# Optimization experiments

Measured on AMD Instinct MI355X. Metric: run time of the kernel, lower is better.

## Reference

```python
import jax, jax.numpy as jnp
import numpy as np

B, D, NUM_HOP, NUM_REL = 8192, 512, 8, 2000  # batch, input_dim, num_hop, num_relation
TAU = 1.0


def setup_inputs() -> dict:
    key = jax.random.key(0)
    ks = jax.random.split(key, 7)
    s = 1.0 / np.sqrt(D)  # PyTorch GRU uniform init bound
    return {
        "query": jax.random.normal(ks[0], (B, D), jnp.float32),
        "W_ih": jax.random.uniform(ks[1], (3 * D, D), jnp.float32, -s, s),
        "W_hh": jax.random.uniform(ks[2], (3 * D, D), jnp.float32, -s, s),
        "b_ih": jax.random.uniform(ks[3], (3 * D,), jnp.float32, -s, s),
        "b_hh": jax.random.uniform(ks[4], (3 * D,), jnp.float32, -s, s),
        "relation": jax.random.normal(ks[5], (2 * NUM_REL, D), jnp.float32),
        "eos": jax.random.normal(ks[6], (1, D), jnp.float32),
    }


def gru_cell(x, h, W_ih, W_hh, b_ih, b_hh):
    # PyTorch nn.GRU cell, gate order (r, z, n)
    gi = x @ W_ih.T + b_ih  # [B, 3D]
    gh = h @ W_hh.T + b_hh  # [B, 3D]
    ir, iz, i_n = jnp.split(gi, 3, axis=-1)
    hr, hz, h_n = jnp.split(gh, 3, axis=-1)
    r = jax.nn.sigmoid(ir + hr)
    z = jax.nn.sigmoid(iz + hz)
    n = jnp.tanh(i_n + r * h_n)
    return (1.0 - z) * n + z * h


def reference(query, W_ih, W_hh, b_ih, b_hh, relation, eos):
    # gru over seq [query, eos] starting from h0 = 0; hidden[1:] == final hx for 1 layer
    h0 = jnp.zeros_like(query)
    h1 = gru_cell(query, h0, W_ih, W_hh, b_ih, b_hh)
    hidden = gru_cell(jnp.broadcast_to(eos, query.shape), h1, W_ih, W_hh, b_ih, b_hh)

    def step(h, _):
        score = jnp.einsum('bd,rd->br', h, relation)          # [B, 2R]
        attention = jax.nn.softmax(score / TAU, axis=-1)
        subgoal = jnp.einsum('br,rd->bd', attention, relation)  # [B, D]
        h_new = gru_cell(subgoal, h, W_ih, W_hh, b_ih, b_hh)
        return h_new, subgoal

    _, subgoals = jax.lax.scan(step, hidden, None, length=NUM_HOP)  # [NUM_HOP, B, D]
    subgoals = jnp.moveaxis(subgoals, 0, 1)  # [B, NUM_HOP, D]
    masks = jnp.ones(subgoals.shape[:-1], dtype=bool)
    return subgoals, masks
```

## Files before the change

### kernel.cpp

```cpp
#include <hip/hip_runtime.h>


typedef _Float16 f16;
typedef _Float16 f16x8 __attribute__((ext_vector_type(8)));
typedef _Float16 f16x4 __attribute__((ext_vector_type(4)));
typedef float    f32x4 __attribute__((ext_vector_type(4)));

constexpr int BATCH = 8192;
constexpr int DDIM  = 512;
constexpr int D3    = 1536;
constexpr int NRELT = 4000;
constexpr int NRELP = 4096;
constexpr int NHOP  = 8;

#define MFMA16(a,b,c) __builtin_amdgcn_mfma_f32_16x16x32_f16((a),(b),(c),0,0,0)
#define BAR()   __builtin_amdgcn_s_barrier()
#define FENCE() asm volatile("" ::: "memory")
#define SCHED0() __builtin_amdgcn_sched_barrier(0)
#define VM(n) asm volatile("s_waitcnt vmcnt(" #n ")" ::: "memory")

__device__ __forceinline__ void gll16(const void* g, void* l) {
  __builtin_amdgcn_global_load_lds(
      (const __attribute__((address_space(1))) unsigned int*)g,
      (__attribute__((address_space(3))) unsigned int*)l, 16, 0, 0);
}

__global__ __launch_bounds__(256) void k_split(const float* __restrict__ src,
                                               f16* __restrict__ hi, f16* __restrict__ lo, int n) {
  int i = blockIdx.x * 256 + threadIdx.x;
  if (i >= n) return;
  float v = src[i];
  f16 h = (f16)v;
  hi[i] = h;
  lo[i] = (f16)(v - (float)h);
}

__global__ __launch_bounds__(256) void k_prep_rel(const float* __restrict__ rel,
    f16* __restrict__ rhi, f16* __restrict__ rlo,
    f16* __restrict__ thi, f16* __restrict__ tlo) {
  int i = blockIdx.x * 256 + threadIdx.x;
  if (i >= NRELP * DDIM) return;
  int r = i >> 9, d = i & 511;
  float v = (r < NRELT) ? rel[i] : 0.f;
  f16 h = (f16)v, l = (f16)(v - (float)h);
  rhi[i] = h; rlo[i] = l;
  thi[(size_t)d * NRELP + r] = h;
  tlo[(size_t)d * NRELP + r] = l;
}

__global__ __launch_bounds__(64) void k_gieos(const float* __restrict__ W,
                                              const float* __restrict__ eos,
                                              float* __restrict__ out) {
  int o = blockIdx.x;
  float s = 0.f;
  for (int i = threadIdx.x; i < DDIM; i += 64) s += W[(size_t)o * DDIM + i] * eos[i];
  for (int off = 32; off; off >>= 1) s += __shfl_xor(s, off);
  if (threadIdx.x == 0) out[o] = s;
}

template<int EPI>
__device__ __forceinline__ void gemm_core(
    const f16* __restrict__ Ahi, const f16* __restrict__ Alo, int lda,
    const f16* __restrict__ Bhi, const f16* __restrict__ Blo, int ldb,
    float* __restrict__ Cout, f16* __restrict__ Chi, f16* __restrict__ Clo,
    int ldc, int m0, int n0, int kst, int nt, f16* lds)
{
  const int tid  = threadIdx.x;
  const int lane = tid & 63;
  const int wave = tid >> 6;
  const int wm = wave >> 2;
  const int wn = wave & 3;
  const int rb = lane & 15;
  const int sl = lane >> 4;
  const int srow = lane >> 2;

  auto stage2 = [&](int buf, int p, int k0) {
    const f16* src = (p == 0) ? Ahi : (p == 1) ? Alo : (p == 2) ? Bhi : Blo;
    const int ld   = (p < 2) ? lda : ldb;
    const int base = (p < 2) ? m0 : n0;
    f16* pl = lds + ((buf * 4 + p) << 13);
    #pragma unroll
    for (int c = 0; c < 2; ++c) {
      const int r0 = wave * 16 + c * 128;
      const int lr = r0 + srow;
      const int slot = (lane & 3) ^ ((lr >> 1) & 3);
      gll16(src + (size_t)(base + lr) * ld + k0 + slot * 8, pl + r0 * 32);
    }
  };
  auto rd = [&](int buf, int p, int lr) -> f16x8 {
    const int off = lr * 64 + ((sl ^ ((lr >> 1) & 3)) << 4);
    return *(const f16x8*)((const char*)(lds + ((buf * 4 + p) << 13)) + off);
  };

  stage2(0, 0, kst); stage2(0, 2, kst); stage2(0, 1, kst); stage2(0, 3, kst);

  f32x4 acc[8][4] = {};
  f16x8 ah[8], al[8], bh[4], bl[4];
  const int A0 = wm * 128, B0 = wn * 64;

  for (int t = 0; t < nt; ++t) {
    const int cur = t & 1;
    const int nxt = cur ^ 1;
    const bool more = (t + 1 < nt);
    const int kn = kst + (t + 1) * 32;

    if (more) { stage2(nxt, 0, kn); stage2(nxt, 2, kn); VM(8); } else { VM(4); }
    BAR(); FENCE();
    #pragma unroll
    for (int f = 0; f < 8; ++f) ah[f] = rd(cur, 0, A0 + f * 16 + rb);
    #pragma unroll
    for (int f = 0; f < 4; ++f) bh[f] = rd(cur, 2, B0 + f * 16 + rb);
    __builtin_amdgcn_s_setprio(1);
    #pragma unroll
    for (int m = 0; m < 8; ++m)
      #pragma unroll
      for (int n = 0; n < 4; ++n)
        acc[m][n] = MFMA16(ah[m], bh[n], acc[m][n]);
    __builtin_amdgcn_s_setprio(0);
    SCHED0();

    if (more) { stage2(nxt, 1, kn); VM(8); } else { VM(2); }
    BAR(); FENCE();
    #pragma unroll
    for (int f = 0; f < 8; ++f) al[f] = rd(cur, 1, A0 + f * 16 + rb);
    __builtin_amdgcn_s_setprio(1);
    #pragma unroll
    for (int m = 0; m < 8; ++m)
      #pragma unroll
      for (int n = 0; n < 4; ++n)
        acc[m][n] = MFMA16(al[m], bh[n], acc[m][n]);
    __builtin_amdgcn_s_setprio(0);
    SCHED0();

    if (more) { stage2(nxt, 3, kn); VM(8); } else { VM(0); }
    BAR(); FENCE();
    #pragma unroll
    for (int f = 0; f < 4; ++f) bl[f] = rd(cur, 3, B0 + f * 16 + rb);
    __builtin_amdgcn_s_setprio(1);
    #pragma unroll
    for (int m = 0; m < 8; ++m)
      #pragma unroll
      for (int n = 0; n < 4; ++n)
        acc[m][n] = MFMA16(ah[m], bl[n], acc[m][n]);
    __builtin_amdgcn_s_setprio(0);
    SCHED0();
  }

  #pragma unroll
  for (int fm = 0; fm < 8; ++fm)
    #pragma unroll
    for (int fn = 0; fn < 4; ++fn)
      #pragma unroll
      for (int r = 0; r < 4; ++r) {
        const int gr = m0 + wm * 128 + fm * 16 + sl * 4 + r;
        const int gc = n0 + wn * 64 + fn * 16 + rb;
        const float v = acc[fm][fn][r];
        if constexpr (EPI == 0) {
          Cout[(size_t)gr * ldc + gc] = v;
        } else {
          const f16 vh = (f16)v;
          Chi[(size_t)gr * ldc + gc] = vh;
          Clo[(size_t)gr * ldc + gc] = (f16)(v - (float)vh);
        }
      }
}

template<int EPI, int TM, int TN>
__global__ __launch_bounds__(512, 2)
void k_gemm8(const f16* __restrict__ Ahi, const f16* __restrict__ Alo, int lda,
             const f16* __restrict__ Bhi, const f16* __restrict__ Blo, int ldb,
             float* __restrict__ Cout, f16* __restrict__ Chi, f16* __restrict__ Clo,
             int ldc, int K, int gy)
{
  __shared__ __align__(16) f16 lds[2 * 4 * 256 * 32];
  const int bid = blockIdx.x;
  const int xcd = bid & 7;
  const int j   = bid >> 3;
  const int within = j % (TM * TN);
  const int st  = xcd + 8 * (j / (TM * TN));
  const int nl  = within / TM;
  const int r   = within % TM;
  const int gmx = 32 / TM;
  const int gmn = gy / TN;
  const int z   = st / (gmx * gmn);
  const int rem = st % (gmx * gmn);
  const int bn  = rem / gmx;
  const int bm  = rem % gmx;
  const int m = bm * TM + r;
  const int n = bn * TN + nl;
  float* Co = Cout ? Cout + (size_t)z * BATCH * (size_t)ldc : nullptr;
  gemm_core<EPI>(Ahi, Alo, lda, Bhi, Blo, ldb, Co, Chi, Clo, ldc,
                 m * 256, n * 256, z * K, K / 32, lds);
}

__global__ __launch_bounds__(512, 2)
void k_gemm8_gru(const f16* __restrict__ xhi, const f16* __restrict__ xlo,
                 const f16* __restrict__ hhi, const f16* __restrict__ hlo,
                 const f16* __restrict__ wihhi, const f16* __restrict__ wihlo,
                 const f16* __restrict__ whhhi, const f16* __restrict__ whhlo,
                 float* __restrict__ gi, float* __restrict__ gh)
{
  __shared__ __align__(16) f16 lds[2 * 4 * 256 * 32];
  const int bid = blockIdx.x;
  const int xcd = bid & 7;
  const int j   = bid >> 3;
  const int nl  = j / 8;
  const int r   = j % 8;
  const int bn  = xcd / 4;
  const int bm  = xcd % 4;
  const int m   = bm * 8 + r;
  const int nn  = bn * 6 + nl;
  const bool second = nn >= 6;
  gemm_core<0>(second ? hhi : xhi, second ? hlo : xlo, DDIM,
               second ? whhhi : wihhi, second ? whhlo : wihlo, DDIM,
               second ? gh : gi, nullptr, nullptr, D3,
               m * 256, (second ? nn - 6 : nn) * 256, 0, DDIM / 32, lds);
}

__global__ __launch_bounds__(256)
void k_softmax(f16* __restrict__ Shi, f16* __restrict__ Slo) {
  const int row = blockIdx.x;
  f16* phi = Shi + (size_t)row * NRELP;
  f16* plo = Slo + (size_t)row * NRELP;
  const int tid = threadIdx.x, lane = tid & 63, wv = tid >> 6;
  const int ng = (tid < 232) ? 4 : 3;
  f32x4 v[4];
  float mx = -3.402823e38f;
  #pragma unroll
  for (int i = 0; i < 4; ++i)
    if (i < ng) {
      f16x4 hv = *(const f16x4*)(phi + (tid + 256 * i) * 4);
      f16x4 lv = *(const f16x4*)(plo + (tid + 256 * i) * 4);
      #pragma unroll
      for (int j = 0; j < 4; ++j) v[i][j] = (float)hv[j] + (float)lv[j];
      mx = fmaxf(fmaxf(fmaxf(mx, v[i][0]), fmaxf(v[i][1], v[i][2])), v[i][3]);
    }
  float l = 0.f;
  #pragma unroll
  for (int i = 0; i < 4; ++i)
    if (i < ng)
      l += __expf(v[i][0] - mx) + __expf(v[i][1] - mx)
         + __expf(v[i][2] - mx) + __expf(v[i][3] - mx);
  #pragma unroll
  for (int off = 1; off < 64; off <<= 1) {
    float om = __shfl_xor(mx, off), ol = __shfl_xor(l, off);
    float nm = fmaxf(mx, om);
    l = l * __expf(mx - nm) + ol * __expf(om - nm);
    mx = nm;
  }
  __shared__ float sm[4], slr[4];
  if (lane == 0) { sm[wv] = mx; slr[wv] = l; }
  __syncthreads();
  const float fm = fmaxf(fmaxf(sm[0], sm[1]), fmaxf(sm[2], sm[3]));
  const float fl = slr[0] * __expf(sm[0] - fm) + slr[1] * __expf(sm[1] - fm)
                 + slr[2] * __expf(sm[2] - fm) + slr[3] * __expf(sm[3] - fm);
  const float il = 1.f / fl;
  #pragma unroll
  for (int i = 0; i < 4; ++i)
    if (i < ng) {
      f16x4 oh, ol;
      #pragma unroll
      for (int j = 0; j < 4; ++j) {
        const float pv = __expf(v[i][j] - fm) * il;
        const f16 ph = (f16)pv;
        oh[j] = ph;
        ol[j] = (f16)(pv - (float)ph);
      }
      *(f16x4*)(phi + (tid + 256 * i) * 4) = oh;
      *(f16x4*)(plo + (tid + 256 * i) * 4) = ol;
    }
  if (tid < 24) {
    f16x4 z = {(f16)0.f, (f16)0.f, (f16)0.f, (f16)0.f};
    *(f16x4*)(phi + (1000 + tid) * 4) = z;
    *(f16x4*)(plo + (1000 + tid) * 4) = z;
  }
}

__global__ __launch_bounds__(256)
void k_subred(const float* __restrict__ Cp, float* __restrict__ outp,
              f16* __restrict__ xhi, f16* __restrict__ xlo, int hop) {
  const int idx = blockIdx.x * 256 + threadIdx.x;
  const int b = idx >> 7, d4 = (idx & 127) * 4;
  const size_t o = (size_t)b * DDIM + d4;
  f32x4 s = *(const f32x4*)(Cp + o);
  s += *(const f32x4*)(Cp + (size_t)BATCH * DDIM + o);
  s += *(const f32x4*)(Cp + 2 * (size_t)BATCH * DDIM + o);
  s += *(const f32x4*)(Cp + 3 * (size_t)BATCH * DDIM + o);
  *(f32x4*)(outp + (size_t)b * (NHOP * DDIM) + (size_t)hop * DDIM + d4) = s;
  f16x4 vh, vl;
  #pragma unroll
  for (int j = 0; j < 4; ++j) {
    const f16 ph = (f16)s[j];
    vh[j] = ph;
    vl[j] = (f16)(s[j] - (float)ph);
  }
  *(f16x4*)(xhi + o) = vh;
  *(f16x4*)(xlo + o) = vl;
}

__global__ __launch_bounds__(256)
void k_gates(const float* __restrict__ gi, const float* __restrict__ givec,
             const float* __restrict__ gh,
             const float* __restrict__ bih, const float* __restrict__ bhh,
             const float* __restrict__ hin, float* __restrict__ hout,
             f16* __restrict__ hhi, f16* __restrict__ hlo)
{
  const int idx = blockIdx.x * 256 + threadIdx.x;
  const int b  = idx >> 7;
  const int d4 = (idx & 127) * 4;
  f32x4 ir, iz, inn;
  if (gi) {
    const float* g = gi + (size_t)b * D3 + d4;
    ir  = *(const f32x4*)(g);
    iz  = *(const f32x4*)(g + DDIM);
    inn = *(const f32x4*)(g + 2 * DDIM);
  } else {
    ir  = *(const f32x4*)(givec + d4);
    iz  = *(const f32x4*)(givec + DDIM + d4);
    inn = *(const f32x4*)(givec + 2 * DDIM + d4);
  }
  ir  += *(const f32x4*)(bih + d4);
  iz  += *(const f32x4*)(bih + DDIM + d4);
  inn += *(const f32x4*)(bih + 2 * DDIM + d4);
  f32x4 hr = {0.f, 0.f, 0.f, 0.f}, hz = {0.f, 0.f, 0.f, 0.f}, hn = {0.f, 0.f, 0.f, 0.f};
  if (gh) {
    const float* g = gh + (size_t)b * D3 + d4;
    hr = *(const f32x4*)(g);
    hz = *(const f32x4*)(g + DDIM);
    hn = *(const f32x4*)(g + 2 * DDIM);
  }
  hr += *(const f32x4*)(bhh + d4);
  hz += *(const f32x4*)(bhh + DDIM + d4);
  hn += *(const f32x4*)(bhh + 2 * DDIM + d4);
  f32x4 hp = {0.f, 0.f, 0.f, 0.f};
  if (hin) hp = *(const f32x4*)(hin + (size_t)b * DDIM + d4);
  f32x4 hv; f16x4 vh, vl;
  #pragma unroll
  for (int j = 0; j < 4; ++j) {
    const float r = 1.f / (1.f + __expf(-(ir[j] + hr[j])));
    const float z = 1.f / (1.f + __expf(-(iz[j] + hz[j])));
    const float n = tanhf(inn[j] + r * hn[j]);
    const float h = (1.f - z) * n + z * hp[j];
    hv[j] = h;
    const f16 ph = (f16)h;
    vh[j] = ph;
    vl[j] = (f16)(h - (float)ph);
  }
  *(f32x4*)(hout + (size_t)b * DDIM + d4) = hv;
  *(f16x4*)(hhi + (size_t)b * DDIM + d4) = vh;
  *(f16x4*)(hlo + (size_t)b * DDIM + d4) = vl;
}

__global__ __launch_bounds__(256) void k_ones(float* __restrict__ o, int n) {
  int i = blockIdx.x * 256 + threadIdx.x;
  if (i < n) o[i] = 1.0f;
}

extern "C" void kernel_launch(void* const* d_in, const int* in_sizes, int n_in,
                              void* d_out, int out_size, void* d_ws, size_t ws_size,
                              hipStream_t stream)
{
  const float* query = (const float*)d_in[0];
  const float* W_ih  = (const float*)d_in[1];
  const float* W_hh  = (const float*)d_in[2];
  const float* b_ih  = (const float*)d_in[3];
  const float* b_hh  = (const float*)d_in[4];
  const float* rel   = (const float*)d_in[5];
  const float* eos   = (const float*)d_in[6];
  float* out = (float*)d_out;
  (void)in_sizes; (void)n_in; (void)out_size; (void)ws_size;

  char* w = (char*)d_ws;
  f16* SPhi    = (f16*)w;   w += (size_t)BATCH * NRELP * 2;
  f16* SPlo    = (f16*)w;   w += (size_t)BATCH * NRELP * 2;
  float* Cpart = (float*)w; w += (size_t)4 * BATCH * DDIM * 4;
  float* hbuf  = (float*)w; w += (size_t)BATCH * DDIM * 4;
  f16* h_hi    = (f16*)w;   w += (size_t)BATCH * DDIM * 2;
  f16* h_lo    = (f16*)w;   w += (size_t)BATCH * DDIM * 2;
  f16* x_hi    = (f16*)w;   w += (size_t)BATCH * DDIM * 2;
  f16* x_lo    = (f16*)w;   w += (size_t)BATCH * DDIM * 2;
  f16* wih_hi  = (f16*)w;   w += (size_t)D3 * DDIM * 2;
  f16* wih_lo  = (f16*)w;   w += (size_t)D3 * DDIM * 2;
  f16* whh_hi  = (f16*)w;   w += (size_t)D3 * DDIM * 2;
  f16* whh_lo  = (f16*)w;   w += (size_t)D3 * DDIM * 2;
  f16* rel_hi  = (f16*)w;   w += (size_t)NRELP * DDIM * 2;
  f16* rel_lo  = (f16*)w;   w += (size_t)NRELP * DDIM * 2;
  f16* relT_hi = (f16*)w;   w += (size_t)DDIM * NRELP * 2;
  f16* relT_lo = (f16*)w;   w += (size_t)DDIM * NRELP * 2;
  float* gieos = (float*)w; w += (size_t)D3 * 4;
  float* gi = (float*)SPhi;
  float* gh = (float*)SPhi + (size_t)BATCH * D3;

  k_split<<<(BATCH * DDIM + 255) / 256, 256, 0, stream>>>(query, x_hi, x_lo, BATCH * DDIM);
  k_split<<<(D3 * DDIM + 255) / 256, 256, 0, stream>>>(W_ih, wih_hi, wih_lo, D3 * DDIM);
  k_split<<<(D3 * DDIM + 255) / 256, 256, 0, stream>>>(W_hh, whh_hi, whh_lo, D3 * DDIM);
  k_prep_rel<<<(NRELP * DDIM + 255) / 256, 256, 0, stream>>>(rel, rel_hi, rel_lo, relT_hi, relT_lo);
  k_gieos<<<D3, 64, 0, stream>>>(W_ih, eos, gieos);

  const int ggrid = BATCH * DDIM / 4 / 256;

  k_gemm8<0, 4, 6><<<192, 512, 0, stream>>>(x_hi, x_lo, DDIM, wih_hi, wih_lo, DDIM,
      gi, nullptr, nullptr, D3, DDIM, 6);
  k_gates<<<ggrid, 256, 0, stream>>>(gi, nullptr, nullptr, b_ih, b_hh, nullptr, hbuf, h_hi, h_lo);

  k_gemm8<0, 4, 6><<<192, 512, 0, stream>>>(h_hi, h_lo, DDIM, whh_hi, whh_lo, DDIM,
      gh, nullptr, nullptr, D3, DDIM, 6);
  k_gates<<<ggrid, 256, 0, stream>>>(nullptr, gieos, gh, b_ih, b_hh, hbuf, hbuf, h_hi, h_lo);

  for (int hop = 0; hop < NHOP; ++hop) {
    k_gemm8<1, 8, 8><<<512, 512, 0, stream>>>(h_hi, h_lo, DDIM, rel_hi, rel_lo, DDIM,
        nullptr, SPhi, SPlo, NRELP, DDIM, 16);
    k_softmax<<<BATCH, 256, 0, stream>>>(SPhi, SPlo);
    k_gemm8<0, 8, 2><<<256, 512, 0, stream>>>(SPhi, SPlo, NRELP,
        relT_hi, relT_lo, NRELP, Cpart, nullptr, nullptr, DDIM, 1024, 2);
    k_subred<<<ggrid, 256, 0, stream>>>(Cpart, out, x_hi, x_lo, hop);
    k_gemm8_gru<<<384, 512, 0, stream>>>(x_hi, x_lo, h_hi, h_lo,
        wih_hi, wih_lo, whh_hi, whh_lo, gi, gh);
    k_gates<<<ggrid, 256, 0, stream>>>(gi, nullptr, gh, b_ih, b_hh, hbuf, hbuf, h_hi, h_lo);
  }

  k_ones<<<(BATCH * NHOP + 255) / 256, 256, 0, stream>>>(out + (size_t)BATCH * NHOP * DDIM, BATCH * NHOP);
}
```

Before: 2.971 ms.

## Replace double-buffered split-plane GEMM pipeline with single-buffer K=64 tiles

```diff
diff --git a/kernel.cpp b/kernel.cpp
--- a/kernel.cpp
+++ b/kernel.cpp
@@ -16,7 +16,6 @@
 #define MFMA16(a,b,c) __builtin_amdgcn_mfma_f32_16x16x32_f16((a),(b),(c),0,0,0)
 #define BAR()   __builtin_amdgcn_s_barrier()
 #define FENCE() asm volatile("" ::: "memory")
-#define SCHED0() __builtin_amdgcn_sched_barrier(0)
 #define VM(n) asm volatile("s_waitcnt vmcnt(" #n ")" ::: "memory")
 
 __device__ __forceinline__ void gll16(const void* g, void* l) {
@@ -72,78 +71,63 @@
   const int wn = wave & 3;
   const int rb = lane & 15;
   const int sl = lane >> 4;
-  const int srow = lane >> 2;
-
-  auto stage2 = [&](int buf, int p, int k0) {
+  const int r8 = lane >> 3;
+  const int s8 = (lane & 7) ^ r8;
+
+  auto stagePlane = [&](int p, int k0) {
     const f16* src = (p == 0) ? Ahi : (p == 1) ? Alo : (p == 2) ? Bhi : Blo;
     const int ld   = (p < 2) ? lda : ldb;
     const int base = (p < 2) ? m0 : n0;
-    f16* pl = lds + ((buf * 4 + p) << 13);
+    f16* pl = lds + (p << 14);
     #pragma unroll
-    for (int c = 0; c < 2; ++c) {
-      const int r0 = wave * 16 + c * 128;
-      const int lr = r0 + srow;
-      const int slot = (lane & 3) ^ ((lr >> 1) & 3);
-      gll16(src + (size_t)(base + lr) * ld + k0 + slot * 8, pl + r0 * 32);
+    for (int i = 0; i < 4; ++i) {
+      const int r0 = wave * 8 + i * 64;
+      gll16(src + (size_t)(base + r0 + r8) * ld + k0 + s8 * 8, pl + r0 * 64);
     }
   };
-  auto rd = [&](int buf, int p, int lr) -> f16x8 {
-    const int off = lr * 64 + ((sl ^ ((lr >> 1) & 3)) << 4);
-    return *(const f16x8*)((const char*)(lds + ((buf * 4 + p) << 13)) + off);
+  auto rd = [&](int p, int lr, int kh) -> f16x8 {
+    const int off = lr * 128 + (((sl + kh * 4) ^ (lr & 7)) << 4);
+    return *(const f16x8*)((const char*)(lds + (p << 14)) + off);
   };
-
-  stage2(0, 0, kst); stage2(0, 2, kst); stage2(0, 1, kst); stage2(0, 3, kst);
 
   f32x4 acc[8][4] = {};
   f16x8 ah[8], al[8], bh[4], bl[4];
   const int A0 = wm * 128, B0 = wn * 64;
 
   for (int t = 0; t < nt; ++t) {
-    const int cur = t & 1;
-    const int nxt = cur ^ 1;
-    const bool more = (t + 1 < nt);
-    const int kn = kst + (t + 1) * 32;
-
-    if (more) { stage2(nxt, 0, kn); stage2(nxt, 2, kn); VM(8); } else { VM(4); }
+    const int k0 = kst + t * 64;
+    stagePlane(0, k0); stagePlane(2, k0); stagePlane(1, k0); stagePlane(3, k0);
+    VM(0);
     BAR(); FENCE();
     #pragma unroll
-    for (int f = 0; f < 8; ++f) ah[f] = rd(cur, 0, A0 + f * 16 + rb);
-    #pragma unroll
-    for (int f = 0; f < 4; ++f) bh[f] = rd(cur, 2, B0 + f * 16 + rb);
-    __builtin_amdgcn_s_setprio(1);
-    #pragma unroll
-    for (int m = 0; m < 8; ++m)
-      #pragma unroll
-      for (int n = 0; n < 4; ++n)
-        acc[m][n] = MFMA16(ah[m], bh[n], acc[m][n]);
-    __builtin_amdgcn_s_setprio(0);
-    SCHED0();
-
-    if (more) { stage2(nxt, 1, kn); VM(8); } else { VM(2); }
-    BAR(); FENCE();
-    #pragma unroll
-    for (int f = 0; f < 8; ++f) al[f] = rd(cur, 1, A0 + f * 16 + rb);
-    __builtin_amdgcn_s_setprio(1);
-    #pragma unroll
-    for (int m = 0; m < 8; ++m)
-      #pragma unroll
-      for (int n = 0; n < 4; ++n)
-        acc[m][n] = MFMA16(al[m], bh[n], acc[m][n]);
-    __builtin_amdgcn_s_setprio(0);
-    SCHED0();
-
-    if (more) { stage2(nxt, 3, kn); VM(8); } else { VM(0); }
-    BAR(); FENCE();
-    #pragma unroll
-    for (int f = 0; f < 4; ++f) bl[f] = rd(cur, 3, B0 + f * 16 + rb);
-    __builtin_amdgcn_s_setprio(1);
-    #pragma unroll
-    for (int m = 0; m < 8; ++m)
-      #pragma unroll
-      for (int n = 0; n < 4; ++n)
-        acc[m][n] = MFMA16(ah[m], bl[n], acc[m][n]);
-    __builtin_amdgcn_s_setprio(0);
-    SCHED0();
+    for (int kh = 0; kh < 2; ++kh) {
+      #pragma unroll
+      for (int f = 0; f < 8; ++f) ah[f] = rd(0, A0 + f * 16 + rb, kh);
+      #pragma unroll
+      for (int f = 0; f < 4; ++f) bh[f] = rd(2, B0 + f * 16 + rb, kh);
+      #pragma unroll
+      for (int f = 0; f < 8; ++f) al[f] = rd(1, A0 + f * 16 + rb, kh);
+      #pragma unroll
+      for (int f = 0; f < 4; ++f) bl[f] = rd(3, B0 + f * 16 + rb, kh);
+      __builtin_amdgcn_s_setprio(1);
+      #pragma unroll
+      for (int m = 0; m < 8; ++m)
+        #pragma unroll
+        for (int n = 0; n < 4; ++n)
+          acc[m][n] = MFMA16(ah[m], bh[n], acc[m][n]);
+      #pragma unroll
+      for (int m = 0; m < 8; ++m)
+        #pragma unroll
+        for (int n = 0; n < 4; ++n)
+          acc[m][n] = MFMA16(al[m], bh[n], acc[m][n]);
+      #pragma unroll
+      for (int m = 0; m < 8; ++m)
+        #pragma unroll
+        for (int n = 0; n < 4; ++n)
+          acc[m][n] = MFMA16(ah[m], bl[n], acc[m][n]);
+      __builtin_amdgcn_s_setprio(0);
+    }
+    FENCE(); BAR();
   }
 
   #pragma unroll
@@ -172,7 +156,7 @@
              float* __restrict__ Cout, f16* __restrict__ Chi, f16* __restrict__ Clo,
              int ldc, int K, int gy)
 {
-  __shared__ __align__(16) f16 lds[2 * 4 * 256 * 32];
+  __shared__ __align__(16) f16 lds[4 * 256 * 64];
   const int bid = blockIdx.x;
   const int xcd = bid & 7;
   const int j   = bid >> 3;
@@ -190,7 +174,7 @@
   const int n = bn * TN + nl;
   float* Co = Cout ? Cout + (size_t)z * BATCH * (size_t)ldc : nullptr;
   gemm_core<EPI>(Ahi, Alo, lda, Bhi, Blo, ldb, Co, Chi, Clo, ldc,
-                 m * 256, n * 256, z * K, K / 32, lds);
+                 m * 256, n * 256, z * K, K / 64, lds);
 }
 
 __global__ __launch_bounds__(512, 2)
@@ -200,7 +184,7 @@
                  const f16* __restrict__ whhhi, const f16* __restrict__ whhlo,
                  float* __restrict__ gi, float* __restrict__ gh)
 {
-  __shared__ __align__(16) f16 lds[2 * 4 * 256 * 32];
+  __shared__ __align__(16) f16 lds[4 * 256 * 64];
   const int bid = blockIdx.x;
   const int xcd = bid & 7;
   const int j   = bid >> 3;
@@ -214,7 +198,7 @@
   gemm_core<0>(second ? hhi : xhi, second ? hlo : xlo, DDIM,
                second ? whhhi : wihhi, second ? whhlo : wihlo, DDIM,
                second ? gh : gi, nullptr, nullptr, D3,
-               m * 256, (second ? nn - 6 : nn) * 256, 0, DDIM / 32, lds);
+               m * 256, (second ? nn - 6 : nn) * 256, 0, DDIM / 64, lds);
 }
 
 __global__ __launch_bounds__(256)
```

After: 3.946 ms. +32.8%, slower.
